# Optimization experiments

Hardware: AMD Instinct MI355X
Metric: run time of the kernel (lower is better)

The kernel has to match this reference:

```python
import jax, jax.numpy as jnp
import numpy as np

WIN_H = WIN_W = 7
NUM_HEADS = 6
DIM = 192
HEAD_DIM = DIM // NUM_HEADS
NUM_WIN = 1024
B_ = 8192
N = WIN_H * WIN_W


def _relative_position_index(win_h, win_w):
    coords = np.stack(np.meshgrid(np.arange(win_h), np.arange(win_w), indexing='ij'))  # (2,h,w)
    flat = coords.reshape(2, -1)
    rel = flat[:, :, None] - flat[:, None, :]          # (2, N, N)
    rel = rel.transpose(1, 2, 0).astype(np.int32)      # (N, N, 2)
    rel[:, :, 0] += win_h - 1
    rel[:, :, 1] += win_w - 1
    rel[:, :, 0] *= 2 * win_w - 1
    return rel.sum(-1)                                 # (N, N) in [0, (2h-1)(2w-1))


def setup_inputs() -> dict:
    key = jax.random.key(0)
    ks = jax.random.split(key, 7)
    return {
        'x': jax.random.normal(ks[0], (B_, N, DIM), jnp.float32),
        'mask': jax.random.normal(ks[1], (NUM_WIN, N, N), jnp.float32),
        'qkv_w': jax.random.normal(ks[2], (3 * DIM, DIM), jnp.float32) * 0.02,
        'qkv_b': jax.random.normal(ks[3], (3 * DIM,), jnp.float32) * 0.02,
        'proj_w': jax.random.normal(ks[4], (DIM, DIM), jnp.float32) * 0.02,
        'proj_b': jax.random.normal(ks[5], (DIM,), jnp.float32) * 0.02,
        'rpb_table': jax.random.normal(ks[6], ((2 * WIN_H - 1) * (2 * WIN_W - 1), NUM_HEADS), jnp.float32) * 0.02,
        'rel_index': jnp.asarray(_relative_position_index(WIN_H, WIN_W)),
    }


def reference(x, mask, qkv_w, qkv_b, proj_w, proj_b, rpb_table, rel_index):
    B, n, C = x.shape
    H, hd = NUM_HEADS, HEAD_DIM
    scale = hd ** (-0.5)

    qkv = (x @ qkv_w.T + qkv_b).reshape(B, n, 3, H, hd)
    qkv = jnp.transpose(qkv, (2, 0, 3, 1, 4))          # (3, B, H, N, hd)
    q, k, v = qkv[0], qkv[1], qkv[2]

    attn = jnp.einsum('bhnd,bhmd->bhnm', q * scale, k)  # (B, H, N, N)

    # gathered relative position bias: (N*N,) -> (N, N, H) -> (H, N, N)
    bias = rpb_table[rel_index.reshape(-1)].reshape(n, n, H)
    attn = attn + jnp.transpose(bias, (2, 0, 1))[None]

    num_win = mask.shape[0]
    attn = attn.reshape(B // num_win, num_win, H, n, n) + mask[None, :, None]
    attn = jax.nn.softmax(attn, axis=-1).reshape(B, H, n, n)

    out = jnp.einsum('bhnm,bhmd->bhnd', attn, v)         # (B, H, N, hd)
    out = jnp.transpose(out, (0, 2, 1, 3)).reshape(B, n, H * hd)
    return out @ proj_w.T + proj_b
```

## Files before the change

kernel.cpp:

```cpp
#include <hip/hip_runtime.h>

#define NTOK  49
#define NWIN  1024
#define SCALE 0.17677669529663687f

#define LDS_MSK 102400
#define LDS_BSB 112640
#define SMEM_BYTES 152640

typedef __bf16 bfx8 __attribute__((ext_vector_type(8)));
typedef float  f32x4 __attribute__((ext_vector_type(4)));
typedef unsigned long long ull;
typedef unsigned int uint;

union BF8 { bfx8 v; ull q[2]; };

__device__ __forceinline__ unsigned short f2bf(float f) {
    uint u = __builtin_bit_cast(uint, f);
    u += 0x7fffu + ((u >> 16) & 1u);
    return (unsigned short)(u >> 16);
}
__device__ __forceinline__ float bf2f(uint u16) {
    uint x = (u16 & 0xffffu) << 16;
    return __builtin_bit_cast(float, x);
}
__device__ __forceinline__ ull pack4(f32x4 a) {
    return (ull)f2bf(a[0]) | ((ull)f2bf(a[1]) << 16) |
           ((ull)f2bf(a[2]) << 32) | ((ull)f2bf(a[3]) << 48);
}

extern "C" __global__ void wattn_prep(const float* __restrict__ qkv_w,
                                      const float* __restrict__ proj_w,
                                      const float* __restrict__ rpb,
                                      const int*   __restrict__ rel,
                                      const float* __restrict__ qkv_b,
                                      unsigned short* __restrict__ W1f,
                                      unsigned short* __restrict__ W2p,
                                      float* __restrict__ qkvbs,
                                      unsigned short* __restrict__ biasB)
{
    const int i = blockIdx.x * 256 + threadIdx.x;
    if (i < 110592) {
        const int e = i & 7, l = (i >> 3) & 63, f = i >> 9;
        const int kk = f % 6, oct = f / 6;
        const int R = oct * 16 + (l & 15), C = kk * 32 + (l >> 4) * 8 + e;
        float v = qkv_w[R * 192 + C];
        if (oct < 12) v *= SCALE;
        W1f[i] = f2bf(v);
    }
    if (i < 36864) {
        const int e = i & 7, l = (i >> 3) & 63, f = i >> 9;
        const int c2t = f / 6, H = f % 6;
        const int R = c2t * 16 + (l & 15);
        const int C = H * 32 + (e >> 2) * 16 + (l >> 4) * 4 + (e & 3);
        W2p[i] = f2bf(proj_w[R * 192 + C]);
    }
    if (i < 576) qkvbs[i] = (i < 192) ? qkv_b[i] * SCALE : qkv_b[i];
    if (i < 6 * NTOK * 68) {
        const int h = i / (NTOK * 68), ii = (i / 68) % NTOK, j = i % 68;
        biasB[i] = (j < NTOK) ? f2bf(rpb[rel[ii * NTOK + j] * 6 + h]) : 0;
    }
}

extern "C" __global__ void __launch_bounds__(512, 2)
wattn_fused(const float* __restrict__ x,
            const float* __restrict__ mask,
            const float* __restrict__ proj_b,
            const unsigned short* __restrict__ W1f,
            const unsigned short* __restrict__ W2p,
            const float* __restrict__ qkvbs,
            const unsigned short* __restrict__ biasB,
            float* __restrict__ out)
{
    __shared__ char smem[SMEM_BYTES];
    char* const XB  = smem;
    char* const OBX = smem;
    char* const QBp = smem + 25600;
    char* const KBp = smem + 50176;
    char* const VTp = smem + 74752;
    char* const MSK = smem + LDS_MSK;
    char* const BSB = smem + LDS_BSB;

    const int tid  = threadIdx.x;
    const int wave = tid >> 6;
    const int lane = tid & 63;
    const int g    = lane >> 4;
    const int jn   = lane & 15;
    const int qt   = wave & 3;
    const size_t b = blockIdx.x;

    bfx8 wfp[6];
#pragma unroll
    for (int kk = 0; kk < 6; ++kk)
        wfp[kk] = *(const bfx8*)(W1f + ((size_t)(wave * 6 + kk) * 64 + lane) * 8);

#pragma unroll
    for (int u = 0; u < 3; ++u) {
        const int i = tid + u * 512;
        if (i < 1500)
            *(uint*)(XB + (49 + i / 100) * 400 + (i % 100) * 4) = 0u;
    }
    {
        const float4* xw = (const float4*)(x + b * 9408);
#pragma unroll
        for (int u = 0; u < 5; ++u) {
            const int i = tid + u * 512;
            if (i < 2352) {
                float4 v = xw[i];
                *(ull*)(XB + (i / 48) * 400 + (i % 48) * 8) =
                    (ull)f2bf(v.x) | ((ull)f2bf(v.y) << 16) |
                    ((ull)f2bf(v.z) << 32) | ((ull)f2bf(v.w) << 48);
            }
        }
    }
    {
        const float* mw = mask + (b & (NWIN - 1)) * (NTOK * NTOK);
#pragma unroll
        for (int u = 0; u < 5; ++u) {
            const int i = tid + u * 512;
            if (i < NTOK * NTOK)
                *(float*)(MSK + ((i / 49) * 52 + (i % 49)) * 4) = mw[i];
        }
    }
    {
        const uint* bsrc = (const uint*)biasB;
        uint* bdst = (uint*)BSB;
#pragma unroll
        for (int u = 0; u < 20; ++u) {
            const int i = tid + u * 512;
            if (i < 9996) bdst[i] = bsrc[i];
        }
    }
    __syncthreads();

#pragma unroll
    for (int jj = 0; jj < 4; ++jj) {
        const int oct = wave + 8 * jj;
        bfx8 wf_[6];
#pragma unroll
        for (int kk = 0; kk < 6; ++kk)
            wf_[kk] = (jj == 0) ? wfp[kk]
                    : *(const bfx8*)(W1f + ((size_t)(oct * 6 + kk) * 64 + lane) * 8);
        if (oct < 24) {
            const f32x4 binit = *(const f32x4*)(qkvbs + oct * 16 + 4 * g);
            char* const dst = (oct < 12) ? QBp : KBp;
            const int ct12 = (oct < 12) ? oct : oct - 12;
#pragma unroll
            for (int tt = 0; tt < 4; ++tt) {
                f32x4 acc = binit;
#pragma unroll
                for (int kk = 0; kk < 6; ++kk) {
                    bfx8 xf = *(const bfx8*)(XB + (tt * 16 + jn) * 400 + kk * 64 + g * 16);
                    acc = __builtin_amdgcn_mfma_f32_16x16x32_bf16(wf_[kk], xf, acc, 0, 0, 0);
                }
                *(ull*)(dst + ((tt * 6 + (ct12 >> 1)) * 64 + lane) * 16 + (ct12 & 1) * 8) = pack4(acc);
            }
        } else {
            const float bv = qkvbs[oct * 16 + jn];
            const int ct12 = oct - 24;
#pragma unroll
            for (int tt = 0; tt < 4; ++tt) {
                f32x4 acc = {bv, bv, bv, bv};
#pragma unroll
                for (int kk = 0; kk < 6; ++kk) {
                    bfx8 xf = *(const bfx8*)(XB + (tt * 16 + jn) * 400 + kk * 64 + g * 16);
                    acc = __builtin_amdgcn_mfma_f32_16x16x32_bf16(xf, wf_[kk], acc, 0, 0, 0);
                }
                *(ull*)(VTp + (ct12 * 16 + jn) * 144 + (tt >> 1) * 64 + g * 16 + (tt & 1) * 8) = pack4(acc);
            }
        }
    }
    {
        const int oct = 32 + (wave >> 1);
        const int ct12 = oct - 24;
        const int ttb = (wave & 1) * 2;
        bfx8 wf_[6];
#pragma unroll
        for (int kk = 0; kk < 6; ++kk)
            wf_[kk] = *(const bfx8*)(W1f + ((size_t)(oct * 6 + kk) * 64 + lane) * 8);
        const float bv = qkvbs[oct * 16 + jn];
#pragma unroll
        for (int t2 = 0; t2 < 2; ++t2) {
            const int tt = ttb + t2;
            f32x4 acc = {bv, bv, bv, bv};
#pragma unroll
            for (int kk = 0; kk < 6; ++kk) {
                bfx8 xf = *(const bfx8*)(XB + (tt * 16 + jn) * 400 + kk * 64 + g * 16);
                acc = __builtin_amdgcn_mfma_f32_16x16x32_bf16(xf, wf_[kk], acc, 0, 0, 0);
            }
            *(ull*)(VTp + (ct12 * 16 + jn) * 144 + (tt >> 1) * 64 + g * 16 + (tt & 1) * 8) = pack4(acc);
        }
    }
    __syncthreads();

    const int hh = wave >> 2;
    const int iq = qt * 16 + jn;
    const int ic = iq < NTOK ? iq : NTOK - 1;
    f32x4 mv4[4];
#pragma unroll
    for (int kt = 0; kt < 4; ++kt)
        mv4[kt] = *(const f32x4*)(MSK + ic * 208 + kt * 64 + g * 16);

#pragma unroll
    for (int hl = 0; hl < 3; ++hl) {
        const int H = hh * 3 + hl;
        bfx8 qfr = *(const bfx8*)(QBp + ((qt * 6 + H) * 64 + lane) * 16);
        f32x4 p[4];
#pragma unroll
        for (int kt = 0; kt < 4; ++kt) {
            bfx8 kf = *(const bfx8*)(KBp + ((kt * 6 + H) * 64 + lane) * 16);
            f32x4 z = {0.f, 0.f, 0.f, 0.f};
            p[kt] = __builtin_amdgcn_mfma_f32_16x16x32_bf16(kf, qfr, z, 0, 0, 0);
        }
        float mx = -1e30f;
#pragma unroll
        for (int kt = 0; kt < 4; ++kt) {
            const ull bq = *(const ull*)(BSB + ((size_t)(H * NTOK + ic)) * 136 + kt * 32 + g * 8);
#pragma unroll
            for (int r = 0; r < 4; ++r) {
                const int j = kt * 16 + 4 * g + r;
                const float v = (j < NTOK)
                    ? p[kt][r] + bf2f((uint)(bq >> (16 * r))) + mv4[kt][r] : -1e30f;
                p[kt][r] = v;
                mx = fmaxf(mx, v);
            }
        }
        mx = fmaxf(mx, __shfl_xor(mx, 16));
        mx = fmaxf(mx, __shfl_xor(mx, 32));
        float sum = 0.f;
#pragma unroll
        for (int kt = 0; kt < 4; ++kt)
#pragma unroll
            for (int r = 0; r < 4; ++r) {
                p[kt][r] = __expf(p[kt][r] - mx);
                sum += p[kt][r];
            }
        sum += __shfl_xor(sum, 16);
        sum += __shfl_xor(sum, 32);
        const float inv = 1.f / sum;
        BF8 p01, p23;
        p01.q[0] = pack4(p[0]); p01.q[1] = pack4(p[1]);
        p23.q[0] = pack4(p[2]); p23.q[1] = pack4(p[3]);
#pragma unroll
        for (int ct = 0; ct < 2; ++ct) {
            const int row = H * 32 + ct * 16 + jn;
            bfx8 v0 = *(const bfx8*)(VTp + row * 144 + g * 16);
            bfx8 v1 = *(const bfx8*)(VTp + row * 144 + 64 + g * 16);
            f32x4 o = {0.f, 0.f, 0.f, 0.f};
            o = __builtin_amdgcn_mfma_f32_16x16x32_bf16(v0, p01.v, o, 0, 0, 0);
            o = __builtin_amdgcn_mfma_f32_16x16x32_bf16(v1, p23.v, o, 0, 0, 0);
            *(ull*)(OBX + ((qt * 6 + H) * 64 + lane) * 16 + ct * 8) = pack4(o * inv);
        }
    }

    bfx8 wf2p[6];
#pragma unroll
    for (int H = 0; H < 6; ++H)
        wf2p[H] = *(const bfx8*)(W2p + ((size_t)((wave >> 1) * 6 + H) * 64 + lane) * 8);
    __syncthreads();

    float* outp = out + b * 9408;
#pragma unroll
    for (int t = 0; t < 3; ++t) {
        const int j = wave + 8 * t;
        const int c2t = j >> 1;
        const int qh  = j & 1;
        bfx8 wf2[6];
#pragma unroll
        for (int H = 0; H < 6; ++H)
            wf2[H] = (t == 0) ? wf2p[H]
                   : *(const bfx8*)(W2p + ((size_t)(c2t * 6 + H) * 64 + lane) * 8);
        const f32x4 pb = *(const f32x4*)(proj_b + c2t * 16 + 4 * g);
#pragma unroll
        for (int t2 = 0; t2 < 2; ++t2) {
            const int qt2 = qh * 2 + t2;
            f32x4 acc = pb;
#pragma unroll
            for (int H = 0; H < 6; ++H) {
                bfx8 ob = *(const bfx8*)(OBX + ((qt2 * 6 + H) * 64 + lane) * 16);
                acc = __builtin_amdgcn_mfma_f32_16x16x32_bf16(wf2[H], ob, acc, 0, 0, 0);
            }
            const int tok = qt2 * 16 + jn;
            if (tok < NTOK)
                *(f32x4*)(outp + tok * 192 + c2t * 16 + 4 * g) = acc;
        }
    }
}

extern "C" void kernel_launch(void* const* d_in, const int* in_sizes, int n_in,
                              void* d_out, int out_size, void* d_ws, size_t ws_size,
                              hipStream_t stream) {
    const float* x      = (const float*)d_in[0];
    const float* mask   = (const float*)d_in[1];
    const float* qkv_w  = (const float*)d_in[2];
    const float* qkv_b  = (const float*)d_in[3];
    const float* proj_w = (const float*)d_in[4];
    const float* proj_b = (const float*)d_in[5];
    const float* rpb    = (const float*)d_in[6];
    const int*   rel    = (const int*)d_in[7];
    float* outp = (float*)d_out;

    char* ws = (char*)d_ws;
    unsigned short* W1f   = (unsigned short*)ws;
    unsigned short* W2p   = (unsigned short*)(ws + 221184);
    float* qkvbs          = (float*)(ws + 221184 + 73728);
    unsigned short* biasB = (unsigned short*)(ws + 221184 + 73728 + 2304);

    wattn_prep<<<432, 256, 0, stream>>>(qkv_w, proj_w, rpb, rel, qkv_b,
                                        W1f, W2p, qkvbs, biasB);
    wattn_fused<<<8192, 512, 0, stream>>>(x, mask, proj_b,
                                          W1f, W2p, qkvbs, biasB, outp);
}
```

Baseline: 461.1 us.

## Process two windows per block, prefetch next x during projection, read mask/bias from global

Each block now handles two consecutive windows, launching half as many blocks, and prefetches the second window's x into registers while the first window's output projection runs. The mask and relative-position bias are no longer staged in LDS; they are read directly from global memory, with padded bias columns prefilled with a large negative value so the per-element bound check can be dropped. LDS usage shrinks, which may allow more resident blocks, but the scattered per-lane mask loads from global memory and the serialized two-window loop could add latency.

```diff
diff --git a/kernel.cpp b/kernel.cpp
--- a/kernel.cpp
+++ b/kernel.cpp
@@ -4,9 +4,7 @@
 #define NWIN  1024
 #define SCALE 0.17677669529663687f
 
-#define LDS_MSK 102400
-#define LDS_BSB 112640
-#define SMEM_BYTES 152640
+#define SMEM_BYTES 126976
 
 typedef __bf16 bfx8 __attribute__((ext_vector_type(8)));
 typedef float  f32x4 __attribute__((ext_vector_type(4)));
@@ -58,7 +56,7 @@
     if (i < 576) qkvbs[i] = (i < 192) ? qkv_b[i] * SCALE : qkv_b[i];
     if (i < 6 * NTOK * 68) {
         const int h = i / (NTOK * 68), ii = (i / 68) % NTOK, j = i % 68;
-        biasB[i] = (j < NTOK) ? f2bf(rpb[rel[ii * NTOK + j] * 6 + h]) : 0;
+        biasB[i] = (j < NTOK) ? f2bf(rpb[rel[ii * NTOK + j] * 6 + h]) : f2bf(-1e30f);
     }
 }
 
@@ -74,12 +72,10 @@
 {
     __shared__ char smem[SMEM_BYTES];
     char* const XB  = smem;
-    char* const OBX = smem;
     char* const QBp = smem + 25600;
     char* const KBp = smem + 50176;
     char* const VTp = smem + 74752;
-    char* const MSK = smem + LDS_MSK;
-    char* const BSB = smem + LDS_BSB;
+    char* const OBX = smem + 102400;
 
     const int tid  = threadIdx.x;
     const int wave = tid >> 6;
@@ -87,7 +83,8 @@
     const int g    = lane >> 4;
     const int jn   = lane & 15;
     const int qt   = wave & 3;
-    const size_t b = blockIdx.x;
+    const int hh   = wave >> 2;
+    const size_t b2 = (size_t)blockIdx.x * 2;
 
     bfx8 wfp[6];
 #pragma unroll
@@ -101,7 +98,7 @@
             *(uint*)(XB + (49 + i / 100) * 400 + (i % 100) * 4) = 0u;
     }
     {
-        const float4* xw = (const float4*)(x + b * 9408);
+        const float4* xw = (const float4*)(x + b2 * 9408);
 #pragma unroll
         for (int u = 0; u < 5; ++u) {
             const int i = tid + u * 512;
@@ -113,53 +110,58 @@
             }
         }
     }
-    {
-        const float* mw = mask + (b & (NWIN - 1)) * (NTOK * NTOK);
-#pragma unroll
-        for (int u = 0; u < 5; ++u) {
-            const int i = tid + u * 512;
-            if (i < NTOK * NTOK)
-                *(float*)(MSK + ((i / 49) * 52 + (i % 49)) * 4) = mw[i];
-        }
-    }
-    {
-        const uint* bsrc = (const uint*)biasB;
-        uint* bdst = (uint*)BSB;
-#pragma unroll
-        for (int u = 0; u < 20; ++u) {
-            const int i = tid + u * 512;
-            if (i < 9996) bdst[i] = bsrc[i];
-        }
-    }
     __syncthreads();
 
-#pragma unroll
-    for (int jj = 0; jj < 4; ++jj) {
-        const int oct = wave + 8 * jj;
-        bfx8 wf_[6];
-#pragma unroll
-        for (int kk = 0; kk < 6; ++kk)
-            wf_[kk] = (jj == 0) ? wfp[kk]
-                    : *(const bfx8*)(W1f + ((size_t)(oct * 6 + kk) * 64 + lane) * 8);
-        if (oct < 24) {
-            const f32x4 binit = *(const f32x4*)(qkvbs + oct * 16 + 4 * g);
-            char* const dst = (oct < 12) ? QBp : KBp;
-            const int ct12 = (oct < 12) ? oct : oct - 12;
-#pragma unroll
-            for (int tt = 0; tt < 4; ++tt) {
-                f32x4 acc = binit;
-#pragma unroll
-                for (int kk = 0; kk < 6; ++kk) {
-                    bfx8 xf = *(const bfx8*)(XB + (tt * 16 + jn) * 400 + kk * 64 + g * 16);
-                    acc = __builtin_amdgcn_mfma_f32_16x16x32_bf16(wf_[kk], xf, acc, 0, 0, 0);
-                }
-                *(ull*)(dst + ((tt * 6 + (ct12 >> 1)) * 64 + lane) * 16 + (ct12 & 1) * 8) = pack4(acc);
-            }
-        } else {
+    for (int w = 0; w < 2; ++w) {
+#pragma unroll
+        for (int jj = 0; jj < 4; ++jj) {
+            const int oct = wave + 8 * jj;
+            bfx8 wf_[6];
+#pragma unroll
+            for (int kk = 0; kk < 6; ++kk)
+                wf_[kk] = (jj == 0) ? wfp[kk]
+                        : *(const bfx8*)(W1f + ((size_t)(oct * 6 + kk) * 64 + lane) * 8);
+            if (oct < 24) {
+                const f32x4 binit = *(const f32x4*)(qkvbs + oct * 16 + 4 * g);
+                char* const dst = (oct < 12) ? QBp : KBp;
+                const int ct12 = (oct < 12) ? oct : oct - 12;
+#pragma unroll
+                for (int tt = 0; tt < 4; ++tt) {
+                    f32x4 acc = binit;
+#pragma unroll
+                    for (int kk = 0; kk < 6; ++kk) {
+                        bfx8 xf = *(const bfx8*)(XB + (tt * 16 + jn) * 400 + kk * 64 + g * 16);
+                        acc = __builtin_amdgcn_mfma_f32_16x16x32_bf16(wf_[kk], xf, acc, 0, 0, 0);
+                    }
+                    *(ull*)(dst + ((tt * 6 + (ct12 >> 1)) * 64 + lane) * 16 + (ct12 & 1) * 8) = pack4(acc);
+                }
+            } else {
+                const float bv = qkvbs[oct * 16 + jn];
+                const int ct12 = oct - 24;
+#pragma unroll
+                for (int tt = 0; tt < 4; ++tt) {
+                    f32x4 acc = {bv, bv, bv, bv};
+#pragma unroll
+                    for (int kk = 0; kk < 6; ++kk) {
+                        bfx8 xf = *(const bfx8*)(XB + (tt * 16 + jn) * 400 + kk * 64 + g * 16);
+                        acc = __builtin_amdgcn_mfma_f32_16x16x32_bf16(xf, wf_[kk], acc, 0, 0, 0);
+                    }
+                    *(ull*)(VTp + (ct12 * 16 + jn) * 144 + (tt >> 1) * 64 + g * 16 + (tt & 1) * 8) = pack4(acc);
+                }
+            }
+        }
+        {
+            const int oct = 32 + (wave >> 1);
+            const int ct12 = oct - 24;
+            const int ttb = (wave & 1) * 2;
+            bfx8 wf_[6];
+#pragma unroll
+            for (int kk = 0; kk < 6; ++kk)
+                wf_[kk] = *(const bfx8*)(W1f + ((size_t)(oct * 6 + kk) * 64 + lane) * 8);
             const float bv = qkvbs[oct * 16 + jn];
-            const int ct12 = oct - 24;
-#pragma unroll
-            for (int tt = 0; tt < 4; ++tt) {
+#pragma unroll
+            for (int t2 = 0; t2 < 2; ++t2) {
+                const int tt = ttb + t2;
                 f32x4 acc = {bv, bv, bv, bv};
 #pragma unroll
                 for (int kk = 0; kk < 6; ++kk) {
@@ -169,120 +171,127 @@
                 *(ull*)(VTp + (ct12 * 16 + jn) * 144 + (tt >> 1) * 64 + g * 16 + (tt & 1) * 8) = pack4(acc);
             }
         }
-    }
-    {
-        const int oct = 32 + (wave >> 1);
-        const int ct12 = oct - 24;
-        const int ttb = (wave & 1) * 2;
-        bfx8 wf_[6];
-#pragma unroll
-        for (int kk = 0; kk < 6; ++kk)
-            wf_[kk] = *(const bfx8*)(W1f + ((size_t)(oct * 6 + kk) * 64 + lane) * 8);
-        const float bv = qkvbs[oct * 16 + jn];
-#pragma unroll
-        for (int t2 = 0; t2 < 2; ++t2) {
-            const int tt = ttb + t2;
-            f32x4 acc = {bv, bv, bv, bv};
-#pragma unroll
-            for (int kk = 0; kk < 6; ++kk) {
-                bfx8 xf = *(const bfx8*)(XB + (tt * 16 + jn) * 400 + kk * 64 + g * 16);
-                acc = __builtin_amdgcn_mfma_f32_16x16x32_bf16(xf, wf_[kk], acc, 0, 0, 0);
-            }
-            *(ull*)(VTp + (ct12 * 16 + jn) * 144 + (tt >> 1) * 64 + g * 16 + (tt & 1) * 8) = pack4(acc);
-        }
-    }
-    __syncthreads();
-
-    const int hh = wave >> 2;
-    const int iq = qt * 16 + jn;
-    const int ic = iq < NTOK ? iq : NTOK - 1;
-    f32x4 mv4[4];
-#pragma unroll
-    for (int kt = 0; kt < 4; ++kt)
-        mv4[kt] = *(const f32x4*)(MSK + ic * 208 + kt * 64 + g * 16);
-
-#pragma unroll
-    for (int hl = 0; hl < 3; ++hl) {
-        const int H = hh * 3 + hl;
-        bfx8 qfr = *(const bfx8*)(QBp + ((qt * 6 + H) * 64 + lane) * 16);
-        f32x4 p[4];
-#pragma unroll
-        for (int kt = 0; kt < 4; ++kt) {
-            bfx8 kf = *(const bfx8*)(KBp + ((kt * 6 + H) * 64 + lane) * 16);
-            f32x4 z = {0.f, 0.f, 0.f, 0.f};
-            p[kt] = __builtin_amdgcn_mfma_f32_16x16x32_bf16(kf, qfr, z, 0, 0, 0);
-        }
-        float mx = -1e30f;
-#pragma unroll
-        for (int kt = 0; kt < 4; ++kt) {
-            const ull bq = *(const ull*)(BSB + ((size_t)(H * NTOK + ic)) * 136 + kt * 32 + g * 8);
+        __syncthreads();
+
+        const int iq = qt * 16 + jn;
+        const int ic = iq < NTOK ? iq : NTOK - 1;
+        const float* mw = mask + ((b2 + w) & (NWIN - 1)) * (NTOK * NTOK);
+        float mv[4][4];
+#pragma unroll
+        for (int kt = 0; kt < 4; ++kt)
 #pragma unroll
             for (int r = 0; r < 4; ++r) {
                 const int j = kt * 16 + 4 * g + r;
-                const float v = (j < NTOK)
-                    ? p[kt][r] + bf2f((uint)(bq >> (16 * r))) + mv4[kt][r] : -1e30f;
-                p[kt][r] = v;
-                mx = fmaxf(mx, v);
-            }
-        }
-        mx = fmaxf(mx, __shfl_xor(mx, 16));
-        mx = fmaxf(mx, __shfl_xor(mx, 32));
-        float sum = 0.f;
-#pragma unroll
-        for (int kt = 0; kt < 4; ++kt)
-#pragma unroll
-            for (int r = 0; r < 4; ++r) {
-                p[kt][r] = __expf(p[kt][r] - mx);
-                sum += p[kt][r];
-            }
-        sum += __shfl_xor(sum, 16);
-        sum += __shfl_xor(sum, 32);
-        const float inv = 1.f / sum;
-        BF8 p01, p23;
-        p01.q[0] = pack4(p[0]); p01.q[1] = pack4(p[1]);
-        p23.q[0] = pack4(p[2]); p23.q[1] = pack4(p[3]);
-#pragma unroll
-        for (int ct = 0; ct < 2; ++ct) {
-            const int row = H * 32 + ct * 16 + jn;
-            bfx8 v0 = *(const bfx8*)(VTp + row * 144 + g * 16);
-            bfx8 v1 = *(const bfx8*)(VTp + row * 144 + 64 + g * 16);
-            f32x4 o = {0.f, 0.f, 0.f, 0.f};
-            o = __builtin_amdgcn_mfma_f32_16x16x32_bf16(v0, p01.v, o, 0, 0, 0);
-            o = __builtin_amdgcn_mfma_f32_16x16x32_bf16(v1, p23.v, o, 0, 0, 0);
-            *(ull*)(OBX + ((qt * 6 + H) * 64 + lane) * 16 + ct * 8) = pack4(o * inv);
-        }
-    }
-
-    bfx8 wf2p[6];
-#pragma unroll
-    for (int H = 0; H < 6; ++H)
-        wf2p[H] = *(const bfx8*)(W2p + ((size_t)((wave >> 1) * 6 + H) * 64 + lane) * 8);
-    __syncthreads();
-
-    float* outp = out + b * 9408;
-#pragma unroll
-    for (int t = 0; t < 3; ++t) {
-        const int j = wave + 8 * t;
-        const int c2t = j >> 1;
-        const int qh  = j & 1;
-        bfx8 wf2[6];
+                const int jc = j < NTOK ? j : NTOK - 1;
+                mv[kt][r] = mw[ic * NTOK + jc];
+            }
+
+#pragma unroll
+        for (int hl = 0; hl < 3; ++hl) {
+            const int H = hh * 3 + hl;
+            bfx8 qfr = *(const bfx8*)(QBp + ((qt * 6 + H) * 64 + lane) * 16);
+            f32x4 p[4];
+#pragma unroll
+            for (int kt = 0; kt < 4; ++kt) {
+                bfx8 kf = *(const bfx8*)(KBp + ((kt * 6 + H) * 64 + lane) * 16);
+                f32x4 z = {0.f, 0.f, 0.f, 0.f};
+                p[kt] = __builtin_amdgcn_mfma_f32_16x16x32_bf16(kf, qfr, z, 0, 0, 0);
+            }
+            float mx = -1e30f;
+#pragma unroll
+            for (int kt = 0; kt < 4; ++kt) {
+                const ull bq = *(const ull*)(biasB + (size_t)(H * NTOK + ic) * 68 + kt * 16 + 4 * g);
+#pragma unroll
+                for (int r = 0; r < 4; ++r) {
+                    const float v = p[kt][r] + bf2f((uint)(bq >> (16 * r))) + mv[kt][r];
+                    p[kt][r] = v;
+                    mx = fmaxf(mx, v);
+                }
+            }
+            mx = fmaxf(mx, __shfl_xor(mx, 16));
+            mx = fmaxf(mx, __shfl_xor(mx, 32));
+            float sum = 0.f;
+#pragma unroll
+            for (int kt = 0; kt < 4; ++kt)
+#pragma unroll
+                for (int r = 0; r < 4; ++r) {
+                    p[kt][r] = __expf(p[kt][r] - mx);
+                    sum += p[kt][r];
+                }
+            sum += __shfl_xor(sum, 16);
+            sum += __shfl_xor(sum, 32);
+            const float inv = 1.f / sum;
+            BF8 p01, p23;
+            p01.q[0] = pack4(p[0]); p01.q[1] = pack4(p[1]);
+            p23.q[0] = pack4(p[2]); p23.q[1] = pack4(p[3]);
+#pragma unroll
+            for (int ct = 0; ct < 2; ++ct) {
+                const int row = H * 32 + ct * 16 + jn;
+                bfx8 v0 = *(const bfx8*)(VTp + row * 144 + g * 16);
+                bfx8 v1 = *(const bfx8*)(VTp + row * 144 + 64 + g * 16);
+                f32x4 o = {0.f, 0.f, 0.f, 0.f};
+                o = __builtin_amdgcn_mfma_f32_16x16x32_bf16(v0, p01.v, o, 0, 0, 0);
+                o = __builtin_amdgcn_mfma_f32_16x16x32_bf16(v1, p23.v, o, 0, 0, 0);
+                *(ull*)(OBX + ((qt * 6 + H) * 64 + lane) * 16 + ct * 8) = pack4(o * inv);
+            }
+        }
+
+        bfx8 wf2p[6];
 #pragma unroll
         for (int H = 0; H < 6; ++H)
-            wf2[H] = (t == 0) ? wf2p[H]
-                   : *(const bfx8*)(W2p + ((size_t)(c2t * 6 + H) * 64 + lane) * 8);
-        const f32x4 pb = *(const f32x4*)(proj_b + c2t * 16 + 4 * g);
-#pragma unroll
-        for (int t2 = 0; t2 < 2; ++t2) {
-            const int qt2 = qh * 2 + t2;
-            f32x4 acc = pb;
-#pragma unroll
-            for (int H = 0; H < 6; ++H) {
-                bfx8 ob = *(const bfx8*)(OBX + ((qt2 * 6 + H) * 64 + lane) * 16);
-                acc = __builtin_amdgcn_mfma_f32_16x16x32_bf16(wf2[H], ob, acc, 0, 0, 0);
-            }
-            const int tok = qt2 * 16 + jn;
-            if (tok < NTOK)
-                *(f32x4*)(outp + tok * 192 + c2t * 16 + 4 * g) = acc;
+            wf2p[H] = *(const bfx8*)(W2p + ((size_t)((wave >> 1) * 6 + H) * 64 + lane) * 8);
+        __syncthreads();
+
+        float4 xr[5];
+        if (w == 0) {
+            const float4* xw1 = (const float4*)(x + (b2 + 1) * 9408);
+#pragma unroll
+            for (int u = 0; u < 5; ++u) {
+                const int i = tid + u * 512;
+                xr[u] = (i < 2352) ? xw1[i] : (float4){0.f, 0.f, 0.f, 0.f};
+            }
+        }
+        float* outp = out + (b2 + w) * 9408;
+#pragma unroll
+        for (int t = 0; t < 3; ++t) {
+            const int j = wave + 8 * t;
+            const int c2t = j >> 1;
+            const int qh  = j & 1;
+            bfx8 wf2[6];
+#pragma unroll
+            for (int H = 0; H < 6; ++H)
+                wf2[H] = (t == 0) ? wf2p[H]
+                       : *(const bfx8*)(W2p + ((size_t)(c2t * 6 + H) * 64 + lane) * 8);
+            const f32x4 pb = *(const f32x4*)(proj_b + c2t * 16 + 4 * g);
+#pragma unroll
+            for (int t2 = 0; t2 < 2; ++t2) {
+                const int qt2 = qh * 2 + t2;
+                f32x4 acc = pb;
+#pragma unroll
+                for (int H = 0; H < 6; ++H) {
+                    bfx8 ob = *(const bfx8*)(OBX + ((qt2 * 6 + H) * 64 + lane) * 16);
+                    acc = __builtin_amdgcn_mfma_f32_16x16x32_bf16(wf2[H], ob, acc, 0, 0, 0);
+                }
+                const int tok = qt2 * 16 + jn;
+                if (tok < NTOK)
+                    *(f32x4*)(outp + tok * 192 + c2t * 16 + 4 * g) = acc;
+            }
+        }
+        if (w == 0) {
+#pragma unroll
+            for (int u = 0; u < 5; ++u) {
+                const int i = tid + u * 512;
+                if (i < 2352) {
+                    float4 v = xr[u];
+                    *(ull*)(XB + (i / 48) * 400 + (i % 48) * 8) =
+                        (ull)f2bf(v.x) | ((ull)f2bf(v.y) << 16) |
+                        ((ull)f2bf(v.z) << 32) | ((ull)f2bf(v.w) << 48);
+                }
+            }
+#pragma unroll
+            for (int kk = 0; kk < 6; ++kk)
+                wfp[kk] = *(const bfx8*)(W1f + ((size_t)(wave * 6 + kk) * 64 + lane) * 8);
+            __syncthreads();
         }
     }
 }
@@ -308,6 +317,6 @@
 
     wattn_prep<<<432, 256, 0, stream>>>(qkv_w, proj_w, rpb, rel, qkv_b,
                                         W1f, W2p, qkvbs, biasB);
-    wattn_fused<<<8192, 512, 0, stream>>>(x, mask, proj_b,
+    wattn_fused<<<4096, 512, 0, stream>>>(x, mask, proj_b,
                                           W1f, W2p, qkvbs, biasB, outp);
 }
```

Result: slower. 1.074 ms (+133.0%).
